# Optimization experiments

Hardware: AMD Instinct MI355X
Metric: run time of the kernel (lower is better)

The kernel has to match this reference:

```python
import jax, jax.numpy as jnp
import numpy as np

T, BS, N = 256, 512, 2048
FUDGE = 1e-4


def setup_inputs() -> dict:
    key = jax.random.key(0)
    ks = jax.random.split(key, 6)
    f32 = jnp.float32
    return {
        "noises": jax.random.normal(ks[0], (T, BS), f32) * 0.1,  # per-step process noise [T, bs]
        "ys": jax.random.normal(ks[1], (T,), f32),               # per-step scalar targets
        "qs": jax.random.normal(ks[2], (T,), f32),               # per-step scalar context input
        "z_biases": jax.random.normal(ks[3], (N,), f32),         # random-feature bias directions
        "w_in": jax.random.normal(ks[4], (N,), f32),             # random input weights
        "w_inq": jax.random.normal(ks[5], (N,), f32),            # random q-input weights
        # scalar learned params (legacy init values)
        "log_learning_rate": jnp.array(-6.0, f32),
        "log_learning_rate_decay": jnp.array(0.0, f32),
        "sigma_b": jnp.array(0.1, f32),
        "output_scale": jnp.array(1.0, f32),
        "u_feedback_scale": jnp.array(1.0, f32),
        "log_weight_decay": jnp.array(-0.001, f32),
        "q_scale": jnp.array(1.0, f32),
        "tauqlpf_m1": jnp.array(-1.0, f32),
        "tauylpf_m1": jnp.array(-1.0, f32),
    }


def _forward(noises, ys, qs, z_biases, w_in, w_inq,
             log_learning_rate, log_learning_rate_decay, sigma_b,
             output_scale, u_feedback_scale, log_weight_decay, q_scale,
             tauqlpf_m1, tauylpf_m1):
    bs = noises.shape[1]
    n = w_in.shape[0]
    softplus = lambda v: jnp.log1p(jnp.exp(v))
    biases = sigma_b * z_biases                    # [n]
    lr0 = jnp.exp(log_learning_rate)               # scalar
    tauq = 1.0 + softplus(tauqlpf_m1)
    tauy = 1.0 + softplus(tauylpf_m1)
    wd = jnp.exp(log_weight_decay)                 # tie_lr_weight_decay=False -> scalar decay
    lr_decay_rate = jnp.exp(log_learning_rate_decay)

    def step(carry, inp):
        w_out, u, e, lr_mult, qlp, ylp = carry
        y, noise_x, q = inp
        qlp = (1.0 - tauq) * qlp + tauq * q
        q_in = w_inq * (q_scale * qlp)             # [n]
        x = u * u_feedback_scale + e + noise_x     # noise injected at node 'x'; [bs]
        h = jax.nn.relu(biases[None, :] + x[:, None] * w_in[None, :] + q_in[None, :])  # [bs, n]
        u = jnp.einsum('kj,kj->k', w_out, h)       # [bs]
        a_mean = output_scale * u                  # [bs]
        # y observed every step (no None/NaN branch)
        ylp = (1.0 - tauy) * ylp + tauy * y
        e = ylp - u                                # [bs]
        lr = lr0 * lr_mult                         # [bs]
        dw = e[:, None] * h * lr[:, None]          # [bs, n]
        w_out = w_out + dw
        norms = jnp.sqrt(FUDGE + jnp.sum(dw * dw, axis=1))
        lr_mult = lr_mult * jnp.exp(-lr_decay_rate * norms)
        w_out = wd * w_out
        return (w_out, u, e, lr_mult, qlp, ylp), a_mean

    init = (jnp.zeros((bs, n), noises.dtype),
            jnp.zeros((bs,), noises.dtype),
            jnp.zeros((bs,), noises.dtype),
            jnp.ones((bs,), noises.dtype),
            jnp.zeros((), noises.dtype),
            jnp.zeros((), noises.dtype))
    _, a_means = jax.lax.scan(step, init, (ys, noises, qs))
    return a_means  # [T, bs]


def reference(noises, ys, qs, z_biases, w_in, w_inq,
              log_learning_rate, log_learning_rate_decay, sigma_b,
              output_scale, u_feedback_scale, log_weight_decay, q_scale,
              tauqlpf_m1, tauylpf_m1):
    return _forward(noises, ys, qs, z_biases, w_in, w_inq,
                    log_learning_rate, log_learning_rate_decay, sigma_b,
                    output_scale, u_feedback_scale, log_weight_decay, q_scale,
                    tauqlpf_m1, tauylpf_m1)
```

## Files before the change

kernel.cpp:

```cpp
#include <hip/hip_runtime.h>
#include <math.h>

#define T_STEPS 256
#define BS      512
#define N       2048
#define BLOCK   64
#define EPT     (N / BLOCK)
#define NP      (EPT / 2)
#define NQ      (EPT / 4)
#define FUDGE   1e-4f

typedef float v2f __attribute__((ext_vector_type(2)));
typedef float v4f __attribute__((ext_vector_type(4)));

__device__ __forceinline__ v2f pk_fma(v2f a, v2f b, v2f c) {
    v2f d;
    asm("v_pk_fma_f32 %0, %1, %2, %3" : "=v"(d) : "v"(a), "v"(b), "v"(c));
    return d;
}
__device__ __forceinline__ v2f pk_add(v2f a, v2f b) {
    v2f d;
    asm("v_pk_add_f32 %0, %1, %2" : "=v"(d) : "v"(a), "v"(b));
    return d;
}

template <int CTRL>
__device__ __forceinline__ float dpp_add(float v) {
    int sh = __builtin_amdgcn_update_dpp(0, __float_as_int(v), CTRL, 0xf, 0xf, true);
    return v + __int_as_float(sh);
}

__device__ __forceinline__ float wave_sum_lane63(float v) {
    v = dpp_add<0x111>(v);
    v = dpp_add<0x112>(v);
    v = dpp_add<0x114>(v);
    v = dpp_add<0x118>(v);
    v = dpp_add<0x142>(v);
    v = dpp_add<0x143>(v);
    return v;
}

__device__ __forceinline__ float bcast63(float v) {
    return __int_as_float(__builtin_amdgcn_readlane(__float_as_int(v), 63));
}

__global__ __launch_bounds__(BLOCK, 1)
void legacy_elbo_scan_kernel(
    const float* __restrict__ noises,
    const float* __restrict__ ys,
    const float* __restrict__ qs,
    const float* __restrict__ z_biases,
    const float* __restrict__ w_in,
    const float* __restrict__ w_inq,
    const float* __restrict__ p_llr,
    const float* __restrict__ p_llrd,
    const float* __restrict__ p_sigb,
    const float* __restrict__ p_oscale,
    const float* __restrict__ p_ufs,
    const float* __restrict__ p_lwd,
    const float* __restrict__ p_qscale,
    const float* __restrict__ p_tauq,
    const float* __restrict__ p_tauy,
    float* __restrict__ out)
{
    const int tid = threadIdx.x;
    const int blk = blockIdx.x;

    __shared__ float ys_s[T_STEPS];
    __shared__ float qs_s[T_STEPS];
    __shared__ float nz_s[T_STEPS];

    for (int i = tid; i < T_STEPS; i += BLOCK) {
        ys_s[i] = ys[i];
        qs_s[i] = qs[i];
        nz_s[i] = noises[i * BS + blk];
    }

    const float sigb    = p_sigb[0];
    const float llr     = p_llr[0];
    const float llrd    = p_llrd[0];
    const float oscale  = p_oscale[0];
    const float ufs     = p_ufs[0];
    const float lwd     = p_lwd[0];
    const float qscale  = p_qscale[0];
    const float tauq_m1 = p_tauq[0];
    const float tauy_m1 = p_tauy[0];

    const float lr0      = expf(llr);
    const float lr_decay = expf(llrd);
    const float wd       = expf(lwd);
    const float rwd      = 1.0f / wd;
    const float tauq     = 1.0f + log1pf(expf(tauq_m1));
    const float tauy     = 1.0f + log1pf(expf(tauy_m1));
    const float omtq     = 1.0f - tauq;
    const float omty     = 1.0f - tauy;

    const v4f* zb4 = (const v4f*)z_biases;
    const v4f* wi4 = (const v4f*)w_in;
    const v4f* wq4 = (const v4f*)w_inq;
    v2f cb[NP], cw[NP], cq[NP];
#pragma unroll
    for (int c = 0; c < NQ; ++c) {
        const int idx = tid + c * BLOCK;
        v4f b = zb4[idx];
        b *= sigb;
        v4f w = wi4[idx];
        v4f g = wq4[idx];
        cb[2*c]   = (v2f){b.x, b.y};  cb[2*c+1] = (v2f){b.z, b.w};
        cw[2*c]   = (v2f){w.x, w.y};  cw[2*c+1] = (v2f){w.z, w.w};
        cq[2*c]   = (v2f){g.x, g.y};  cq[2*c+1] = (v2f){g.z, g.w};
    }

    v2f v[NP];
#pragma unroll
    for (int i = 0; i < NP; ++i) v[i] = (v2f){0.0f, 0.0f};

    float u = 0.0f, e = 0.0f, lr_mult = 1.0f, qlp = 0.0f, ylp = 0.0f;
    float sp = 1.0f, rsp = 1.0f;

    __syncthreads();

    float q_c = qs_s[0], y_c = ys_s[0], n_c = nz_s[0];

    for (int t = 0; t < T_STEPS; ++t) {
        const int tn = (t + 1 < T_STEPS) ? t + 1 : t;
        const float q_n = qs_s[tn], y_n = ys_s[tn], n_n = nz_s[tn];

        qlp = omtq * qlp + tauq * q_c;
        const float qsc = qscale * qlp;
        const float x   = fmaf(u, ufs, e) + n_c;
        const v2f xx = (v2f){x, x};
        const v2f qq = (v2f){qsc, qsc};

        v2f h[NP];
        v2f su_a[4], sh_a[4];
#pragma unroll
        for (int a = 0; a < 4; ++a) {
            su_a[a] = (v2f){0.0f, 0.0f};
            sh_a[a] = (v2f){0.0f, 0.0f};
        }
#pragma unroll
        for (int i = 0; i < NP; ++i) {
            v2f t2 = pk_fma(qq, cq[i], cb[i]);
            t2 = pk_fma(xx, cw[i], t2);
            v2f hh;
            hh.x = fmaxf(t2.x, 0.0f);
            hh.y = fmaxf(t2.y, 0.0f);
            h[i] = hh;
            su_a[i & 3] = pk_fma(v[i], hh, su_a[i & 3]);
            sh_a[i & 3] = pk_fma(hh, hh, sh_a[i & 3]);
        }
        v2f su2 = pk_add(pk_add(su_a[0], su_a[1]), pk_add(su_a[2], su_a[3]));
        v2f sh2 = pk_add(pk_add(sh_a[0], sh_a[1]), pk_add(sh_a[2], sh_a[3]));
        float su_l = su2.x + su2.y;
        float sh_l = sh2.x + sh2.y;

        const float su_w = wave_sum_lane63(su_l);
        const float sh_w = wave_sum_lane63(sh_l);
        const float su_t = bcast63(su_w);
        const float sh_t = bcast63(sh_w);

        u = sp * su_t;
        if (tid == 0) out[t * BS + blk] = oscale * u;

        ylp = omty * ylp + tauy * y_c;
        e = ylp - u;
        const float el = e * (lr0 * lr_mult);
        const float c  = el * rsp;
        const v2f cc = (v2f){c, c};

#pragma unroll
        for (int i = 0; i < NP; ++i)
            v[i] = pk_fma(cc, h[i], v[i]);

        const float nrm = sqrtf(fmaf(el * el, sh_t, FUDGE));
        lr_mult *= __expf(-lr_decay * nrm);
        sp  *= wd;
        rsp *= rwd;

        q_c = q_n; y_c = y_n; n_c = n_n;
    }
}

extern "C" void kernel_launch(void* const* d_in, const int* in_sizes, int n_in,
                              void* d_out, int out_size, void* d_ws, size_t ws_size,
                              hipStream_t stream) {
    (void)in_sizes; (void)n_in; (void)d_ws; (void)ws_size; (void)out_size;
    const float* noises   = (const float*)d_in[0];
    const float* ys       = (const float*)d_in[1];
    const float* qs       = (const float*)d_in[2];
    const float* z_biases = (const float*)d_in[3];
    const float* w_in     = (const float*)d_in[4];
    const float* w_inq    = (const float*)d_in[5];
    const float* llr      = (const float*)d_in[6];
    const float* llrd     = (const float*)d_in[7];
    const float* sigb     = (const float*)d_in[8];
    const float* oscale   = (const float*)d_in[9];
    const float* ufs      = (const float*)d_in[10];
    const float* lwd      = (const float*)d_in[11];
    const float* qscale   = (const float*)d_in[12];
    const float* tauq     = (const float*)d_in[13];
    const float* tauy     = (const float*)d_in[14];
    float* out = (float*)d_out;

    hipLaunchKernelGGL(legacy_elbo_scan_kernel, dim3(BS), dim3(BLOCK), 0, stream,
                       noises, ys, qs, z_biases, w_in, w_inq,
                       llr, llrd, sigb, oscale, ufs, lwd, qscale, tauq, tauy,
                       out);
}
```

Measured before the change: 222.3 us.

## Split each batch row across two waves with LDS cross-wave reduction

Doubles the block to 128 threads so each batch row's 2048 features are split across two wavefronts, halving the per-thread register state and serial work per step. The per-wave sums are combined through a double-buffered shared-memory array with a __syncthreads each timestep. The packed v_pk_fma inline asm is replaced by scalar fmaf, relying on the compiler to pack. The trade is a block barrier and an LDS round trip on every step of the serial scan.

```diff
diff --git a/kernel.cpp b/kernel.cpp
--- a/kernel.cpp
+++ b/kernel.cpp
@@ -4,25 +4,11 @@
 #define T_STEPS 256
 #define BS      512
 #define N       2048
-#define BLOCK   64
+#define BLOCK   128
+#define NWAVE   (BLOCK / 64)
 #define EPT     (N / BLOCK)
-#define NP      (EPT / 2)
 #define NQ      (EPT / 4)
 #define FUDGE   1e-4f
-
-typedef float v2f __attribute__((ext_vector_type(2)));
-typedef float v4f __attribute__((ext_vector_type(4)));
-
-__device__ __forceinline__ v2f pk_fma(v2f a, v2f b, v2f c) {
-    v2f d;
-    asm("v_pk_fma_f32 %0, %1, %2, %3" : "=v"(d) : "v"(a), "v"(b), "v"(c));
-    return d;
-}
-__device__ __forceinline__ v2f pk_add(v2f a, v2f b) {
-    v2f d;
-    asm("v_pk_add_f32 %0, %1, %2" : "=v"(d) : "v"(a), "v"(b));
-    return d;
-}
 
 template <int CTRL>
 __device__ __forceinline__ float dpp_add(float v) {
@@ -40,11 +26,7 @@
     return v;
 }
 
-__device__ __forceinline__ float bcast63(float v) {
-    return __int_as_float(__builtin_amdgcn_readlane(__float_as_int(v), 63));
-}
-
-__global__ __launch_bounds__(BLOCK, 1)
+__global__ __launch_bounds__(BLOCK, 2)
 void legacy_elbo_scan_kernel(
     const float* __restrict__ noises,
     const float* __restrict__ ys,
@@ -63,12 +45,15 @@
     const float* __restrict__ p_tauy,
     float* __restrict__ out)
 {
-    const int tid = threadIdx.x;
-    const int blk = blockIdx.x;
+    const int tid  = threadIdx.x;
+    const int wid  = tid >> 6;
+    const int lane = tid & 63;
+    const int blk  = blockIdx.x;
 
     __shared__ float ys_s[T_STEPS];
     __shared__ float qs_s[T_STEPS];
     __shared__ float nz_s[T_STEPS];
+    __shared__ __align__(16) float red[2][4];
 
     for (int i = tid; i < T_STEPS; i += BLOCK) {
         ys_s[i] = ys[i];
@@ -95,25 +80,23 @@
     const float omtq     = 1.0f - tauq;
     const float omty     = 1.0f - tauy;
 
-    const v4f* zb4 = (const v4f*)z_biases;
-    const v4f* wi4 = (const v4f*)w_in;
-    const v4f* wq4 = (const v4f*)w_inq;
-    v2f cb[NP], cw[NP], cq[NP];
+    const float4* zb4 = (const float4*)z_biases;
+    const float4* wi4 = (const float4*)w_in;
+    const float4* wq4 = (const float4*)w_inq;
+    float4 cb_r[NQ], cw_r[NQ], cq_r[NQ];
 #pragma unroll
     for (int c = 0; c < NQ; ++c) {
         const int idx = tid + c * BLOCK;
-        v4f b = zb4[idx];
-        b *= sigb;
-        v4f w = wi4[idx];
-        v4f g = wq4[idx];
-        cb[2*c]   = (v2f){b.x, b.y};  cb[2*c+1] = (v2f){b.z, b.w};
-        cw[2*c]   = (v2f){w.x, w.y};  cw[2*c+1] = (v2f){w.z, w.w};
-        cq[2*c]   = (v2f){g.x, g.y};  cq[2*c+1] = (v2f){g.z, g.w};
+        float4 b = zb4[idx];
+        b.x *= sigb; b.y *= sigb; b.z *= sigb; b.w *= sigb;
+        cb_r[c] = b;
+        cw_r[c] = wi4[idx];
+        cq_r[c] = wq4[idx];
     }
 
-    v2f v[NP];
+    float v[EPT];
 #pragma unroll
-    for (int i = 0; i < NP; ++i) v[i] = (v2f){0.0f, 0.0f};
+    for (int i = 0; i < EPT; ++i) v[i] = 0.0f;
 
     float u = 0.0f, e = 0.0f, lr_mult = 1.0f, qlp = 0.0f, ylp = 0.0f;
     float sp = 1.0f, rsp = 1.0f;
@@ -129,36 +112,40 @@
         qlp = omtq * qlp + tauq * q_c;
         const float qsc = qscale * qlp;
         const float x   = fmaf(u, ufs, e) + n_c;
-        const v2f xx = (v2f){x, x};
-        const v2f qq = (v2f){qsc, qsc};
 
-        v2f h[NP];
-        v2f su_a[4], sh_a[4];
+        float su0 = 0.f, su1 = 0.f, sh0 = 0.f, sh1 = 0.f;
+        float h[EPT];
 #pragma unroll
-        for (int a = 0; a < 4; ++a) {
-            su_a[a] = (v2f){0.0f, 0.0f};
-            sh_a[a] = (v2f){0.0f, 0.0f};
+        for (int c = 0; c < NQ; ++c) {
+            const float4 b4 = cb_r[c];
+            const float4 w4 = cw_r[c];
+            const float4 g4 = cq_r[c];
+            float h0 = fmaxf(fmaf(x, w4.x, fmaf(qsc, g4.x, b4.x)), 0.0f);
+            float h1 = fmaxf(fmaf(x, w4.y, fmaf(qsc, g4.y, b4.y)), 0.0f);
+            float h2 = fmaxf(fmaf(x, w4.z, fmaf(qsc, g4.z, b4.z)), 0.0f);
+            float h3 = fmaxf(fmaf(x, w4.w, fmaf(qsc, g4.w, b4.w)), 0.0f);
+            h[4*c+0] = h0; h[4*c+1] = h1; h[4*c+2] = h2; h[4*c+3] = h3;
+            su0 = fmaf(v[4*c+0], h0, su0);
+            su1 = fmaf(v[4*c+1], h1, su1);
+            su0 = fmaf(v[4*c+2], h2, su0);
+            su1 = fmaf(v[4*c+3], h3, su1);
+            sh0 = fmaf(h0, h0, sh0);
+            sh1 = fmaf(h1, h1, sh1);
+            sh0 = fmaf(h2, h2, sh0);
+            sh1 = fmaf(h3, h3, sh1);
         }
-#pragma unroll
-        for (int i = 0; i < NP; ++i) {
-            v2f t2 = pk_fma(qq, cq[i], cb[i]);
-            t2 = pk_fma(xx, cw[i], t2);
-            v2f hh;
-            hh.x = fmaxf(t2.x, 0.0f);
-            hh.y = fmaxf(t2.y, 0.0f);
-            h[i] = hh;
-            su_a[i & 3] = pk_fma(v[i], hh, su_a[i & 3]);
-            sh_a[i & 3] = pk_fma(hh, hh, sh_a[i & 3]);
+        const float su_w = wave_sum_lane63(su0 + su1);
+        const float sh_w = wave_sum_lane63(sh0 + sh1);
+
+        const int p = t & 1;
+        if (lane == 63) {
+            red[p][wid * 2]     = su_w;
+            red[p][wid * 2 + 1] = sh_w;
         }
-        v2f su2 = pk_add(pk_add(su_a[0], su_a[1]), pk_add(su_a[2], su_a[3]));
-        v2f sh2 = pk_add(pk_add(sh_a[0], sh_a[1]), pk_add(sh_a[2], sh_a[3]));
-        float su_l = su2.x + su2.y;
-        float sh_l = sh2.x + sh2.y;
-
-        const float su_w = wave_sum_lane63(su_l);
-        const float sh_w = wave_sum_lane63(sh_l);
-        const float su_t = bcast63(su_w);
-        const float sh_t = bcast63(sh_w);
+        __syncthreads();
+        const float4 r = *(const float4*)&red[p][0];
+        const float su_t = r.x + r.z;
+        const float sh2  = r.y + r.w;
 
         u = sp * su_t;
         if (tid == 0) out[t * BS + blk] = oscale * u;
@@ -167,13 +154,12 @@
         e = ylp - u;
         const float el = e * (lr0 * lr_mult);
         const float c  = el * rsp;
-        const v2f cc = (v2f){c, c};
 
 #pragma unroll
-        for (int i = 0; i < NP; ++i)
-            v[i] = pk_fma(cc, h[i], v[i]);
+        for (int i = 0; i < EPT; ++i)
+            v[i] = fmaf(c, h[i], v[i]);
 
-        const float nrm = sqrtf(fmaf(el * el, sh_t, FUDGE));
+        const float nrm = sqrtf(fmaf(el * el, sh2, FUDGE));
         lr_mult *= __expf(-lr_decay * nrm);
         sp  *= wd;
         rsp *= rwd;
```

After: 242.9 us. 1.09x slower.
